# Performance work log

Hardware: AMD Instinct MI355X
Metric: run time of the kernel (lower is better)

Reference implementation:

```python
import jax, jax.numpy as jnp
import numpy as np

VOCAB = 32000
EMBED = 512
UNITS = 64  # LSTM hidden size hardcoded in the source
B, T = 32, 128
T_ENC = 128


def setup_inputs() -> dict:
    key = jax.random.key(0)
    ks = jax.random.split(key, 10)
    decoder_inputs = jax.random.randint(ks[0], (B, T), 0, VOCAB)
    encoder_inputs = jax.random.normal(ks[1], (B, T_ENC, UNITS), jnp.float32)
    h0 = 0.1 * jax.random.normal(ks[2], (B, UNITS), jnp.float32)
    c0 = 0.1 * jax.random.normal(ks[3], (B, UNITS), jnp.float32)
    emb = 0.02 * jax.random.normal(ks[4], (VOCAB, EMBED), jnp.float32)
    Wx = 0.05 * jax.random.normal(ks[5], (EMBED, 4 * UNITS), jnp.float32)
    Wh = 0.05 * jax.random.normal(ks[6], (UNITS, 4 * UNITS), jnp.float32)
    # keras unit_forget_bias=True: forget-gate bias initialized to 1
    b = jnp.zeros((4 * UNITS,), jnp.float32).at[UNITS:2 * UNITS].set(1.0)
    Wd = 0.02 * jax.random.normal(ks[7], (2 * UNITS, VOCAB), jnp.float32)
    bd = jnp.zeros((VOCAB,), jnp.float32)
    return {"encoder_inputs": encoder_inputs, "decoder_inputs": decoder_inputs,
            "h0": h0, "c0": c0, "emb": emb, "Wx": Wx, "Wh": Wh, "b": b,
            "Wd": Wd, "bd": bd}


def reference(encoder_inputs, decoder_inputs, h0, c0, emb, Wx, Wh, b, Wd, bd):
    # Embedding (dropout layers are identity at inference)
    x = emb[decoder_inputs]                      # [B, T, E]
    # Precompute input contribution to all gates for all timesteps
    xz = jnp.einsum('bte,eg->btg', x, Wx) + b    # [B, T, 4U]

    def step(carry, zt):
        h, c = carry
        z = zt + h @ Wh                           # [B, 4U]
        i, f, g, o = jnp.split(z, 4, axis=-1)     # keras gate order i,f,c,o
        i = jax.nn.sigmoid(i)
        f = jax.nn.sigmoid(f)
        o = jax.nn.sigmoid(o)
        c_new = f * c + i * jnp.tanh(g)
        h_new = o * jnp.tanh(c_new)
        return (h_new, c_new), h_new

    (hT, cT), hs = jax.lax.scan(step, (h0, c0), jnp.swapaxes(xz, 0, 1))
    seq = jnp.swapaxes(hs, 0, 1)                  # [B, T, U]

    # key_value = concat(h0, seq[:, :-1])  -> queries for Luong attention
    kv = jnp.concatenate([h0[:, None, :], seq[:, :-1, :]], axis=1)  # [B, T, U]
    # keras Attention([q, v]): scores = q @ v^T, softmax, ctx = attn @ v
    scores = jnp.einsum('btu,bsu->bts', kv, encoder_inputs)         # [B, T, T_enc]
    attn = jax.nn.softmax(scores, axis=-1)
    ctx = jnp.einsum('bts,bsu->btu', attn, encoder_inputs)          # [B, T, U]

    feat = jnp.concatenate([seq, ctx], axis=-1)   # [B, T, 2U]
    out = jax.nn.softmax(jnp.einsum('btu,uv->btv', feat, Wd) + bd, axis=-1)
    return out, hT, cT
```

## Files before the change

kernel.cpp:

```cpp
#include <hip/hip_runtime.h>
#include <hip/hip_bf16.h>
#include <math.h>

#define B_   32
#define T_   128
#define TE_  128
#define U_   64
#define E_   512
#define V_   32000
#define G_   256

typedef __attribute__((ext_vector_type(8))) short  short8x;
typedef __attribute__((ext_vector_type(4))) float  f32x4;
typedef __attribute__((ext_vector_type(4))) unsigned short u16x4;

__device__ inline unsigned short f2bf(float x) {
    union { float f; unsigned int u; } v; v.f = x;
    unsigned int u = v.u;
    u = (u + 0x7FFFu + ((u >> 16) & 1u)) >> 16;
    return (unsigned short)u;
}

__global__ void embed_xz_kernel(const int* __restrict__ dec,
                                const float* __restrict__ emb,
                                const float* __restrict__ Wx,
                                const float* __restrict__ bias,
                                float* __restrict__ xz) {
    __shared__ float xs[16][E_];
    int tid = threadIdx.x;
    int rb = blockIdx.x * 16;
#pragma unroll
    for (int i = 0; i < 8; i++) {
        int idx = tid + i * 256;
        int r = idx >> 7, q = idx & 127;
        ((float4*)xs[r])[q] = ((const float4*)(emb + (size_t)dec[rb + r] * E_))[q];
    }
    __syncthreads();
    float acc[16];
#pragma unroll
    for (int r = 0; r < 16; r++) acc[r] = 0.f;
    for (int e = 0; e < E_; e++) {
        float w = Wx[e * G_ + tid];
#pragma unroll
        for (int r = 0; r < 16; r++) acc[r] += xs[r][e] * w;
    }
    float bv = bias[tid];
#pragma unroll
    for (int r = 0; r < 16; r++)
        xz[(size_t)(rb + r) * G_ + tid] = acc[r] + bv;
}

__global__ void lstm_kernel(const float* __restrict__ xz,
                            const float* __restrict__ h0,
                            const float* __restrict__ c0,
                            const float* __restrict__ Wh,
                            float* __restrict__ feat,
                            float* __restrict__ hT,
                            float* __restrict__ cT) {
    int b = blockIdx.x;
    int g = threadIdx.x;
    float w[U_];
#pragma unroll
    for (int u = 0; u < U_; u++) w[u] = Wh[u * G_ + g];
    __shared__ float h[U_];
    __shared__ float c[U_];
    __shared__ float z[G_];
    if (g < U_) { h[g] = h0[b * U_ + g]; c[g] = c0[b * U_ + g]; }
    __syncthreads();
    const float* xzb = xz + (size_t)b * T_ * G_;
    for (int t = 0; t < T_; t++) {
        float acc = xzb[t * G_ + g];
#pragma unroll
        for (int u = 0; u < U_; u++) acc += h[u] * w[u];
        z[g] = acc;
        __syncthreads();
        if (g < U_) {
            float iv = 1.f / (1.f + expf(-z[g]));
            float fv = 1.f / (1.f + expf(-z[U_ + g]));
            float gv = tanhf(z[2 * U_ + g]);
            float ov = 1.f / (1.f + expf(-z[3 * U_ + g]));
            float cn = fv * c[g] + iv * gv;
            float hn = ov * tanhf(cn);
            c[g] = cn; h[g] = hn;
            feat[((size_t)b * T_ + t) * 2 * U_ + g] = hn;
        }
        __syncthreads();
    }
    if (g < U_) { hT[b * U_ + g] = h[g]; cT[b * U_ + g] = c[g]; }
}

__global__ void attn_kernel(const float* __restrict__ enc,
                            const float* __restrict__ h0,
                            float* __restrict__ feat) {
    int row = blockIdx.x;
    int b = row >> 7;
    int t = row & (T_ - 1);
    int tid = threadIdx.x;
    __shared__ float kv[U_];
    __shared__ float at[TE_];
    __shared__ float red[TE_];
    if (tid < U_)
        kv[tid] = (t == 0) ? h0[b * U_ + tid] : feat[(size_t)(row - 1) * 2 * U_ + tid];
    __syncthreads();
    const float* encb = enc + (size_t)b * TE_ * U_;
    float s = 0.f;
    const float4* e4 = (const float4*)(encb + tid * U_);
#pragma unroll
    for (int u4 = 0; u4 < U_ / 4; u4++) {
        float4 ev = e4[u4];
        s += ev.x * kv[u4 * 4 + 0] + ev.y * kv[u4 * 4 + 1] +
             ev.z * kv[u4 * 4 + 2] + ev.w * kv[u4 * 4 + 3];
    }
    red[tid] = s;
    __syncthreads();
    for (int off = 64; off > 0; off >>= 1) {
        if (tid < off) red[tid] = fmaxf(red[tid], red[tid + off]);
        __syncthreads();
    }
    float m = red[0];
    __syncthreads();
    float e = expf(s - m);
    at[tid] = e;
    red[tid] = e;
    __syncthreads();
    for (int off = 64; off > 0; off >>= 1) {
        if (tid < off) red[tid] += red[tid + off];
        __syncthreads();
    }
    float inv_sum = 1.f / red[0];
    __syncthreads();
    if (tid < U_) {
        float cacc = 0.f;
#pragma unroll 4
        for (int sx = 0; sx < TE_; sx++)
            cacc += at[sx] * encb[sx * U_ + tid];
        feat[(size_t)row * 2 * U_ + U_ + tid] = cacc * inv_sum;
    }
}

__global__ void feat_to_bf16(const float* __restrict__ feat,
                             unsigned short* __restrict__ fb) {
    int i = blockIdx.x * 256 + threadIdx.x;
    float4 v = ((const float4*)feat)[i];
    u16x4 o;
    o.x = f2bf(v.x); o.y = f2bf(v.y); o.z = f2bf(v.z); o.w = f2bf(v.w);
    *(u16x4*)(fb + (size_t)i * 4) = o;
}

__global__ void wd_transpose(const float* __restrict__ Wd,
                             unsigned short* __restrict__ wdt) {
    __shared__ float t[128][65];
    int tid = threadIdx.x;
    int nb = blockIdx.x * 64;
#pragma unroll
    for (int i = 0; i < 32; i++) {
        int idx = tid + i * 256;
        int k = idx >> 6, n = idx & 63;
        t[k][n] = Wd[(size_t)k * V_ + nb + n];
    }
    __syncthreads();
    int n = tid >> 2, kq = tid & 3;
#pragma unroll
    for (int g = 0; g < 4; g++) {
        short8x s;
#pragma unroll
        for (int j = 0; j < 8; j++)
            s[j] = (short)f2bf(t[kq * 32 + g * 8 + j][n]);
        *(short8x*)(wdt + (size_t)(nb + n) * 128 + kq * 32 + g * 8) = s;
    }
}

__global__ void gemm_stats(const unsigned short* __restrict__ fb,
                           const unsigned short* __restrict__ wdt,
                           const float* __restrict__ bd,
                           float* __restrict__ partial) {
    int tid = threadIdx.x;
    int lane = tid & 63, wave = tid >> 6;
    int lrow = lane & 15, quad = lane >> 4;
    int rowbase = blockIdx.x * 64 + wave * 16;
    int cb = blockIdx.y;
    int col0 = cb * 1280;

    short8x a[4];
    const unsigned short* ap = fb + (size_t)(rowbase + lrow) * 128 + quad * 8;
#pragma unroll
    for (int k = 0; k < 4; k++) a[k] = *(const short8x*)(ap + k * 32);

    float s[4] = {0.f, 0.f, 0.f, 0.f};
    for (int ch = 0; ch < 10; ch++) {
        int cc = col0 + ch * 128;
        f32x4 acc[8];
#pragma unroll
        for (int ct = 0; ct < 8; ct++) acc[ct] = {0.f, 0.f, 0.f, 0.f};
        const unsigned short* bp = wdt + (size_t)(cc + lrow) * 128 + quad * 8;
#pragma unroll
        for (int ct = 0; ct < 8; ct++) {
#pragma unroll
            for (int k = 0; k < 4; k++) {
                short8x b = *(const short8x*)(bp + (size_t)ct * 16 * 128 + k * 32);
                acc[ct] = __builtin_amdgcn_mfma_f32_16x16x32_bf16(a[k], b, acc[ct], 0, 0, 0);
            }
        }
#pragma unroll
        for (int ct = 0; ct < 8; ct++) {
            float bdv = bd[cc + ct * 16 + lrow];
#pragma unroll
            for (int r = 0; r < 4; r++)
                s[r] += __expf(acc[ct][r] + bdv);
        }
    }
#pragma unroll
    for (int r = 0; r < 4; r++) {
        float v = s[r];
        v += __shfl_xor(v, 1);
        v += __shfl_xor(v, 2);
        v += __shfl_xor(v, 4);
        v += __shfl_xor(v, 8);
        if (lrow == 0)
            partial[(size_t)(rowbase + quad * 4 + r) * 25 + cb] = v;
    }
}

__global__ void merge_stats(const float* __restrict__ partial,
                            float* __restrict__ inv_s) {
    int r = blockIdx.x * 256 + threadIdx.x;
    float s = 0.f;
#pragma unroll
    for (int i = 0; i < 25; i++) s += partial[(size_t)r * 25 + i];
    inv_s[r] = 1.f / s;
}

__global__ void gemm_norm(const unsigned short* __restrict__ fb,
                          const unsigned short* __restrict__ wdt,
                          const float* __restrict__ bd,
                          const float* __restrict__ inv_s,
                          float* __restrict__ out) {
    __shared__ float lds[64 * 132];
    int tid = threadIdx.x;
    int lane = tid & 63, wave = tid >> 6;
    int lrow = lane & 15, quad = lane >> 4;
    int rowblk = blockIdx.x * 64;
    int rowbase = rowblk + wave * 16;
    int col0 = blockIdx.y * 1280;

    short8x a[4];
    const unsigned short* ap = fb + (size_t)(rowbase + lrow) * 128 + quad * 8;
#pragma unroll
    for (int k = 0; k < 4; k++) a[k] = *(const short8x*)(ap + k * 32);

    float inv[4];
#pragma unroll
    for (int r = 0; r < 4; r++) inv[r] = inv_s[rowbase + quad * 4 + r];

    for (int ch = 0; ch < 10; ch++) {
        int cc = col0 + ch * 128;
        f32x4 acc[8];
#pragma unroll
        for (int ct = 0; ct < 8; ct++) acc[ct] = {0.f, 0.f, 0.f, 0.f};
        const unsigned short* bp = wdt + (size_t)(cc + lrow) * 128 + quad * 8;
#pragma unroll
        for (int ct = 0; ct < 8; ct++) {
#pragma unroll
            for (int k = 0; k < 4; k++) {
                short8x b = *(const short8x*)(bp + (size_t)ct * 16 * 128 + k * 32);
                acc[ct] = __builtin_amdgcn_mfma_f32_16x16x32_bf16(a[k], b, acc[ct], 0, 0, 0);
            }
        }
        __syncthreads();
#pragma unroll
        for (int ct = 0; ct < 8; ct++) {
            float bdv = bd[cc + ct * 16 + lrow];
#pragma unroll
            for (int r = 0; r < 4; r++)
                lds[(wave * 16 + quad * 4 + r) * 132 + ct * 16 + lrow] =
                    __expf(acc[ct][r] + bdv) * inv[r];
        }
        __syncthreads();
#pragma unroll
        for (int i = 0; i < 8; i++) {
            int idx = tid + i * 256;
            int r = idx >> 5, c4 = idx & 31;
            float4 v = *(float4*)&lds[r * 132 + c4 * 4];
            *(float4*)(out + (size_t)(rowblk + r) * V_ + cc + c4 * 4) = v;
        }
    }
}

extern "C" void kernel_launch(void* const* d_in, const int* in_sizes, int n_in,
                              void* d_out, int out_size, void* d_ws, size_t ws_size,
                              hipStream_t stream) {
    const float* enc  = (const float*)d_in[0];
    const int*   dec  = (const int*)d_in[1];
    const float* h0   = (const float*)d_in[2];
    const float* c0   = (const float*)d_in[3];
    const float* emb  = (const float*)d_in[4];
    const float* Wx   = (const float*)d_in[5];
    const float* Wh   = (const float*)d_in[6];
    const float* bias = (const float*)d_in[7];
    const float* Wd   = (const float*)d_in[8];
    const float* bd   = (const float*)d_in[9];
    float* out = (float*)d_out;
    float* ws  = (float*)d_ws;

    const int NROW = B_ * T_;
    float* xz      = ws;
    float* feat    = xz + (size_t)NROW * G_;
    float* partial = feat + (size_t)NROW * 2 * U_;
    float* inv_s   = partial + (size_t)NROW * 25;
    unsigned short* fb  = (unsigned short*)(inv_s + NROW);
    unsigned short* wdt = (unsigned short*)(fb + (size_t)NROW * 2 * U_);
    float* hT = out + (size_t)NROW * V_;
    float* cT = hT + B_ * U_;

    wd_transpose<<<dim3(V_ / 64), 256, 0, stream>>>(Wd, wdt);
    embed_xz_kernel<<<dim3(NROW / 16), 256, 0, stream>>>(dec, emb, Wx, bias, xz);
    lstm_kernel<<<dim3(B_), 256, 0, stream>>>(xz, h0, c0, Wh, feat, hT, cT);
    attn_kernel<<<dim3(NROW), 128, 0, stream>>>(enc, h0, feat);
    feat_to_bf16<<<dim3(NROW * 2 * U_ / 1024), 256, 0, stream>>>(feat, fb);
    gemm_stats<<<dim3(64, 25), 256, 0, stream>>>(fb, wdt, bd, partial);
    merge_stats<<<dim3(NROW / 256), 256, 0, stream>>>(partial, inv_s);
    gemm_norm<<<dim3(64, 25), 256, 0, stream>>>(fb, wdt, bd, inv_s, out);
}
```

Baseline: 1.256 ms.

## Vectorize LDS reads, remap GEMM blocks per XCD, use nontemporal output stores

The embedding projection and the LSTM recurrence now read shared memory as float4 and split each dot product into 4-term partial sums. Both GEMM kernels switch to a 1D grid whose block IDs are remapped so that blocks landing on the same XCD (ID mod 8) handle contiguous tiles and share cached Wd/feature data. The 524 MB softmax output is written with nontemporal stores so it does not evict useful cache lines. Together these aim at LDS instruction count, L2 locality across chiplets, and cache pollution from the large output write.

```diff
diff --git a/kernel.cpp b/kernel.cpp
--- a/kernel.cpp
+++ b/kernel.cpp
@@ -39,10 +39,16 @@
     float acc[16];
 #pragma unroll
     for (int r = 0; r < 16; r++) acc[r] = 0.f;
-    for (int e = 0; e < E_; e++) {
-        float w = Wx[e * G_ + tid];
-#pragma unroll
-        for (int r = 0; r < 16; r++) acc[r] += xs[r][e] * w;
+    for (int e = 0; e < E_; e += 4) {
+        float w0 = Wx[(e + 0) * G_ + tid];
+        float w1 = Wx[(e + 1) * G_ + tid];
+        float w2 = Wx[(e + 2) * G_ + tid];
+        float w3 = Wx[(e + 3) * G_ + tid];
+#pragma unroll
+        for (int r = 0; r < 16; r++) {
+            float4 xv = *(const float4*)&xs[r][e];
+            acc[r] += xv.x * w0 + xv.y * w1 + xv.z * w2 + xv.w * w3;
+        }
     }
     float bv = bias[tid];
 #pragma unroll
@@ -71,7 +77,11 @@
     for (int t = 0; t < T_; t++) {
         float acc = xzb[t * G_ + g];
 #pragma unroll
-        for (int u = 0; u < U_; u++) acc += h[u] * w[u];
+        for (int u4 = 0; u4 < U_ / 4; u4++) {
+            float4 hv = *(const float4*)&h[u4 * 4];
+            acc += hv.x * w[u4 * 4 + 0] + hv.y * w[u4 * 4 + 1] +
+                   hv.z * w[u4 * 4 + 2] + hv.w * w[u4 * 4 + 3];
+        }
         z[g] = acc;
         __syncthreads();
         if (g < U_) {
@@ -170,15 +180,22 @@
     }
 }
 
+__device__ inline void gemm_block_map(int L, int& rowblk, int& colblk) {
+    int W = (L & 7) * 200 + (L >> 3);
+    colblk = W >> 6;
+    rowblk = W & 63;
+}
+
 __global__ void gemm_stats(const unsigned short* __restrict__ fb,
                            const unsigned short* __restrict__ wdt,
                            const float* __restrict__ bd,
                            float* __restrict__ partial) {
+    int rowblk, cb;
+    gemm_block_map(blockIdx.x, rowblk, cb);
     int tid = threadIdx.x;
     int lane = tid & 63, wave = tid >> 6;
     int lrow = lane & 15, quad = lane >> 4;
-    int rowbase = blockIdx.x * 64 + wave * 16;
-    int cb = blockIdx.y;
+    int rowbase = rowblk * 64 + wave * 16;
     int col0 = cb * 1280;
 
     short8x a[4];
@@ -236,12 +253,14 @@
                           const float* __restrict__ inv_s,
                           float* __restrict__ out) {
     __shared__ float lds[64 * 132];
+    int rowblkI, cbI;
+    gemm_block_map(blockIdx.x, rowblkI, cbI);
     int tid = threadIdx.x;
     int lane = tid & 63, wave = tid >> 6;
     int lrow = lane & 15, quad = lane >> 4;
-    int rowblk = blockIdx.x * 64;
+    int rowblk = rowblkI * 64;
     int rowbase = rowblk + wave * 16;
-    int col0 = blockIdx.y * 1280;
+    int col0 = cbI * 1280;
 
     short8x a[4];
     const unsigned short* ap = fb + (size_t)(rowbase + lrow) * 128 + quad * 8;
@@ -280,8 +299,9 @@
         for (int i = 0; i < 8; i++) {
             int idx = tid + i * 256;
             int r = idx >> 5, c4 = idx & 31;
-            float4 v = *(float4*)&lds[r * 132 + c4 * 4];
-            *(float4*)(out + (size_t)(rowblk + r) * V_ + cc + c4 * 4) = v;
+            f32x4 v = *(f32x4*)&lds[r * 132 + c4 * 4];
+            __builtin_nontemporal_store(v,
+                (f32x4*)(out + (size_t)(rowblk + r) * V_ + cc + c4 * 4));
         }
     }
 }
@@ -317,7 +337,7 @@
     lstm_kernel<<<dim3(B_), 256, 0, stream>>>(xz, h0, c0, Wh, feat, hT, cT);
     attn_kernel<<<dim3(NROW), 128, 0, stream>>>(enc, h0, feat);
     feat_to_bf16<<<dim3(NROW * 2 * U_ / 1024), 256, 0, stream>>>(feat, fb);
-    gemm_stats<<<dim3(64, 25), 256, 0, stream>>>(fb, wdt, bd, partial);
+    gemm_stats<<<dim3(1600), 256, 0, stream>>>(fb, wdt, bd, partial);
     merge_stats<<<dim3(NROW / 256), 256, 0, stream>>>(partial, inv_s);
-    gemm_norm<<<dim3(64, 25), 256, 0, stream>>>(fb, wdt, bd, inv_s, out);
-}
+    gemm_norm<<<dim3(1600), 256, 0, stream>>>(fb, wdt, bd, inv_s, out);
+}
```

Measured after the change: 1.222 ms. 1.03x faster.
